# Performance work log

Hardware: AMD Instinct MI355X
Metric: run time of the kernel (lower is better)

Reference implementation:

```python
import jax, jax.numpy as jnp
import numpy as np

B, N_UNITS, SEQ, H = 4, 1024, 2048, 8
D_HEAD = N_UNITS // H
SCALE = 1.0 / D_HEAD ** 0.5


def setup_inputs() -> dict:
    key = jax.random.key(0)
    k1, k2, k3 = jax.random.split(key, 3)
    x = jax.random.normal(k1, (B, N_UNITS, SEQ), dtype=jnp.float32)
    # conv1x1 weights, bias=False; scaled like typical init
    W_qkv = jax.random.normal(k2, (3 * N_UNITS, N_UNITS), dtype=jnp.float32) * (1.0 / N_UNITS ** 0.5)
    W_out = jax.random.normal(k3, (N_UNITS, N_UNITS), dtype=jnp.float32) * (1.0 / N_UNITS ** 0.5)
    return {"x": x, "W_qkv": W_qkv, "W_out": W_out}


def reference(x, W_qkv, W_out):
    # x: (B, n_units, S). Conv1x1 == per-position linear along channel dim.
    qkv = jnp.einsum('oc,bcs->bos', W_qkv, x)          # (B, 3*n_units, S)
    Q, K, V = jnp.split(qkv, 3, axis=1)                # each (B, n_units, S)
    # torch.chunk along channels into h heads == reshape (B, h, d_head, S)
    Q = Q.reshape(B, H, D_HEAD, SEQ)
    K = K.reshape(B, H, D_HEAD, SEQ)
    V = V.reshape(B, H, D_HEAD, SEQ)
    # scores: Q^T K * scale  (NO softmax in original module; mask unused)
    A = jnp.einsum('bhdq,bhdk->bhqk', Q, K) * SCALE    # (B, h, S, S)
    # aggregation: sum_k A[q,k] * V[d,k]  (original does broadcast mul+sum)
    C = jnp.einsum('bhqk,bhdk->bhdq', A, V)            # (B, h, d_head, S)
    C = C.reshape(B, N_UNITS, SEQ)
    out = jnp.einsum('oc,bcs->bos', W_out, C)          # (B, n_units, S)
    return out
```

## Files before the change

### kernel.cpp

```cpp
#include <hip/hip_runtime.h>
#include <hip/hip_bf16.h>
#include <stdint.h>

using bf16 = __hip_bfloat16;

typedef __bf16 bf16x8 __attribute__((ext_vector_type(8)));
typedef float  f32x4  __attribute__((ext_vector_type(4)));

constexpr int Bc = 4, Hh = 8, Dh = 128, S = 2048, Cn = 1024, O3 = 3072;
constexpr float SCALE = 0.08838834764831845f;

#define GLDS16(gp, lp)                                               \
  __builtin_amdgcn_global_load_lds(                                  \
      (const __attribute__((address_space(1))) void*)(gp),           \
      (__attribute__((address_space(3))) void*)(lp), 16, 0, 0)

__device__ __forceinline__ void gemm_bt_core(
    const bf16* __restrict__ Abase, int lda,
    const bf16* __restrict__ Bbase, int ldb,
    int kIters, f32x4 (&acc)[4][4])
{
  alignas(16) __shared__ bf16 As[128 * 32];
  alignas(16) __shared__ bf16 Bs[128 * 32];
  const int t    = threadIdx.x;
  const int lane = t & 63;
  const int quad = lane >> 4, r16 = lane & 15;
  const int wave = t >> 6;
  const int wm = (wave & 1) * 64, wn = (wave >> 1) * 64;
  const int lrow = lane >> 2;
  const int lk   = (lane & 3) * 8;

  const long aOff0 = (long)(wave * 32 + lrow) * lda + lk;
  const long aOff1 = aOff0 + 16l * lda;
  const long bOff0 = (long)(wave * 32 + lrow) * ldb + lk;
  const long bOff1 = bOff0 + 16l * ldb;
  bf16* aL0 = &As[(wave * 32) * 32];
  bf16* aL1 = &As[(wave * 32 + 16) * 32];
  bf16* bL0 = &Bs[(wave * 32) * 32];
  bf16* bL1 = &Bs[(wave * 32 + 16) * 32];

#pragma unroll
  for (int i = 0; i < 4; i++)
#pragma unroll
    for (int j = 0; j < 4; j++) acc[i][j] = {0.f, 0.f, 0.f, 0.f};

  for (int ks = 0; ks < kIters; ++ks) {
    const int k0 = ks * 32;
    __syncthreads();
    GLDS16(Abase + k0 + aOff0, aL0);
    GLDS16(Abase + k0 + aOff1, aL1);
    GLDS16(Bbase + k0 + bOff0, bL0);
    GLDS16(Bbase + k0 + bOff1, bL1);
    __syncthreads();
    bf16x8 af[4], bfr[4];
#pragma unroll
    for (int i = 0; i < 4; i++)
      af[i] = *(const bf16x8*)&As[(wm + i * 16 + r16) * 32 + quad * 8];
#pragma unroll
    for (int j = 0; j < 4; j++)
      bfr[j] = *(const bf16x8*)&Bs[(wn + j * 16 + r16) * 32 + quad * 8];
#pragma unroll
    for (int i = 0; i < 4; i++)
#pragma unroll
      for (int j = 0; j < 4; j++)
        acc[i][j] = __builtin_amdgcn_mfma_f32_16x16x32_bf16(af[i], bfr[j], acc[i][j], 0, 0, 0);
  }
}

__device__ __forceinline__ void store_bf16_tile(
    f32x4 (&acc)[4][4], bf16* __restrict__ Cp, int ldc)
{
  const int t = threadIdx.x;
  const int lane = t & 63;
  const int quad = lane >> 4, r16 = lane & 15;
  const int wave = t >> 6;
  const int wm = (wave & 1) * 64, wn = (wave >> 1) * 64;
#pragma unroll
  for (int i = 0; i < 4; i++)
#pragma unroll
    for (int j = 0; j < 4; j++)
#pragma unroll
      for (int r = 0; r < 4; r++) {
        const int row = wm + i * 16 + quad * 4 + r;
        const int col = wn + j * 16 + r16;
        Cp[(long)row * ldc + col] = __float2bfloat16(acc[i][j][r]);
      }
}

__device__ __forceinline__ void store_f32_tile(
    f32x4 (&acc)[4][4], float* __restrict__ Cp, int ldc)
{
  const int t = threadIdx.x;
  const int lane = t & 63;
  const int quad = lane >> 4, r16 = lane & 15;
  const int wave = t >> 6;
  const int wm = (wave & 1) * 64, wn = (wave >> 1) * 64;
#pragma unroll
  for (int i = 0; i < 4; i++)
#pragma unroll
    for (int j = 0; j < 4; j++)
#pragma unroll
      for (int r = 0; r < 4; r++) {
        const int row = wm + i * 16 + quad * 4 + r;
        const int col = wn + j * 16 + r16;
        Cp[(long)row * ldc + col] = acc[i][j][r];
      }
}

__global__ __launch_bounds__(256) void k_cvt_w(
    const float* __restrict__ Wqkv, const float* __restrict__ Wout,
    bf16* __restrict__ WqkvB, bf16* __restrict__ WoutB)
{
  const long v = (long)blockIdx.x * 256 + threadIdx.x;
  const bool isQ = v < 786432;
  const float4 f = isQ ? ((const float4*)Wqkv)[v] : ((const float4*)Wout)[v - 786432];
  bf16 tmp[4];
  tmp[0] = __float2bfloat16(f.x);
  tmp[1] = __float2bfloat16(f.y);
  tmp[2] = __float2bfloat16(f.z);
  tmp[3] = __float2bfloat16(f.w);
  ushort4 u = *(ushort4*)tmp;
  if (isQ) ((ushort4*)WqkvB)[v] = u;
  else     ((ushort4*)WoutB)[v - 786432] = u;
}

__global__ __launch_bounds__(256) void k_transpose_cvt(
    const float* __restrict__ in, bf16* __restrict__ out, long inZ, long outZ)
{
  __shared__ bf16 tile[32][33];
  const float* ip = in + (long)blockIdx.z * inZ;
  bf16* op = out + (long)blockIdx.z * outZ;
  const int c0 = blockIdx.x * 32, r0 = blockIdx.y * 32;
  const int tx = threadIdx.x & 31, ty = threadIdx.x >> 5;
#pragma unroll
  for (int i = 0; i < 32; i += 8)
    tile[ty + i][tx] = __float2bfloat16(ip[(long)(r0 + ty + i) * 2048 + c0 + tx]);
  __syncthreads();
#pragma unroll
  for (int i = 0; i < 32; i += 8)
    op[(long)(c0 + ty + i) * 1024 + r0 + tx] = tile[tx][ty + i];
}

__global__ __launch_bounds__(256) void k_gemm_qT(
    const bf16* __restrict__ xT, const bf16* __restrict__ WqkvB, bf16* __restrict__ QT)
{
  const int m0 = blockIdx.x * 128, n0 = blockIdx.y * 128, b = blockIdx.z;
  f32x4 acc[4][4];
  gemm_bt_core(xT + (long)b * S * Cn + (long)m0 * Cn, Cn,
               WqkvB + (long)n0 * Cn, Cn, Cn / 32, acc);
  store_bf16_tile(acc, QT + (long)b * S * Cn + (long)m0 * Cn + n0, Cn);
}

__global__ __launch_bounds__(256) void k_gemm_kv(
    const bf16* __restrict__ WqkvB, const bf16* __restrict__ xT, bf16* __restrict__ KV)
{
  const int m0 = blockIdx.x * 128, n0 = blockIdx.y * 128, b = blockIdx.z;
  f32x4 acc[4][4];
  gemm_bt_core(WqkvB + (long)(Cn + m0) * Cn, Cn,
               xT + (long)b * S * Cn + (long)n0 * Cn, Cn, Cn / 32, acc);
  store_bf16_tile(acc, KV + (long)b * 2048 * S + (long)m0 * S + n0, S);
}

__global__ __launch_bounds__(256) void k_gemm_mt(
    const bf16* __restrict__ KV, float* __restrict__ MTpart)
{
  const int chunk = blockIdx.x;
  const int z = blockIdx.y;
  const int b = z >> 3, h = z & 7;
  const bf16* base = KV + (long)b * 2048 * S;
  const bf16* A  = base + (long)(h * Dh) * S + chunk * 256;
  const bf16* Bp = base + (long)(1024 + h * Dh) * S + chunk * 256;
  f32x4 acc[4][4];
  gemm_bt_core(A, S, Bp, S, 8, acc);
  store_f32_tile(acc, MTpart + ((long)chunk * 32 + z) * (Dh * Dh), Dh);
}

__global__ __launch_bounds__(256) void k_reduce_mt(
    const float* __restrict__ MTpart, bf16* __restrict__ MbT)
{
  const long i = (long)blockIdx.x * 256 + threadIdx.x;
  float s = 0.f;
#pragma unroll
  for (int c = 0; c < 8; c++) s += MTpart[(long)c * 32 * Dh * Dh + i];
  MbT[i] = __float2bfloat16(s * SCALE);
}

__global__ __launch_bounds__(256) void k_gemm_w2(
    const bf16* __restrict__ WoutB, const bf16* __restrict__ MbT, bf16* __restrict__ W2)
{
  const int m0 = blockIdx.x * 128;
  const int h = blockIdx.y, b = blockIdx.z;
  const int z = b * 8 + h;
  f32x4 acc[4][4];
  gemm_bt_core(WoutB + (long)m0 * Cn + h * Dh, Cn,
               MbT + (long)z * Dh * Dh, Dh, 4, acc);
  store_bf16_tile(acc, W2 + (long)b * Cn * Cn + (long)m0 * Cn + h * Dh, Cn);
}

__global__ __launch_bounds__(256) void k_gemm_out(
    const bf16* __restrict__ W2, const bf16* __restrict__ QT, float* __restrict__ out)
{
  const int m0 = blockIdx.x * 128, n0 = blockIdx.y * 128, b = blockIdx.z;
  f32x4 acc[4][4];
  gemm_bt_core(W2 + (long)b * Cn * Cn + (long)m0 * Cn, Cn,
               QT + (long)b * S * Cn + (long)n0 * Cn, Cn, Cn / 32, acc);
  store_f32_tile(acc, out + (long)b * Cn * S + (long)m0 * S + n0, S);
}

extern "C" void kernel_launch(void* const* d_in, const int* in_sizes, int n_in,
                              void* d_out, int out_size, void* d_ws, size_t ws_size,
                              hipStream_t stream)
{
  const float* x    = (const float*)d_in[0];
  const float* Wqkv = (const float*)d_in[1];
  const float* Wout = (const float*)d_in[2];
  float* out = (float*)d_out;

  char* ws = (char*)d_ws;
  bf16*  KV     = (bf16*)ws;
  bf16*  xT     = (bf16*)(ws + 33554432);
  float* MTpart = (float*)(ws + 33554432);
  bf16*  QT     = (bf16*)(ws + 50331648);
  bf16*  WqkvB  = (bf16*)(ws + 67108864);
  bf16*  WoutB  = (bf16*)(ws + 73400320);
  bf16*  MbT    = (bf16*)(ws + 75497472);
  bf16*  W2     = (bf16*)(ws + 76546048);

  k_cvt_w<<<dim3(4096), 256, 0, stream>>>(Wqkv, Wout, WqkvB, WoutB);
  k_transpose_cvt<<<dim3(64, 32, 4), 256, 0, stream>>>(
      x, xT, (long)1024 * 2048, (long)2048 * 1024);
  k_gemm_qT<<<dim3(16, 8, 4), 256, 0, stream>>>(xT, WqkvB, QT);
  k_gemm_kv<<<dim3(16, 16, 4), 256, 0, stream>>>(WqkvB, xT, KV);
  k_gemm_mt<<<dim3(8, 32), 256, 0, stream>>>(KV, MTpart);
  k_reduce_mt<<<dim3(2048), 256, 0, stream>>>(MTpart, MbT);
  k_gemm_w2<<<dim3(8, 8, 4), 256, 0, stream>>>(WoutB, MbT, W2);
  k_gemm_out<<<dim3(8, 16, 4), 256, 0, stream>>>(W2, QT, out);
}
```

Baseline: 221.8 us.

## Reassociate attention chain through input Gram matrix to avoid materializing K, V, Q

Replaces the explicit Q/K/V projections with an algebraic reassociation. The per-batch Gram matrix G = x x^T is computed first, then K V^T is formed per head as Wk G Wv^T, and Wout·M is folded with Wq into one per-batch 1024x1024 weight W3 that multiplies x directly. The aim is to cut the large S-dimension GEMMs and the KV intermediate traffic, and to drop the split-K partial-sum reduction kernel. In exchange it adds extra small weight-side GEMMs and rounds G, P and W3 to bf16, which may change accuracy.

```diff
diff --git a/kernel.cpp b/kernel.cpp
--- a/kernel.cpp
+++ b/kernel.cpp
@@ -7,7 +7,7 @@
 typedef __bf16 bf16x8 __attribute__((ext_vector_type(8)));
 typedef float  f32x4  __attribute__((ext_vector_type(4)));
 
-constexpr int Bc = 4, Hh = 8, Dh = 128, S = 2048, Cn = 1024, O3 = 3072;
+constexpr int Dh = 128, S = 2048, Cn = 1024;
 constexpr float SCALE = 0.08838834764831845f;
 
 #define GLDS16(gp, lp)                                               \
@@ -68,7 +68,7 @@
 }
 
 __device__ __forceinline__ void store_bf16_tile(
-    f32x4 (&acc)[4][4], bf16* __restrict__ Cp, int ldc)
+    f32x4 (&acc)[4][4], bf16* __restrict__ Cp, int ldc, float mul = 1.0f)
 {
   const int t = threadIdx.x;
   const int lane = t & 63;
@@ -83,7 +83,7 @@
       for (int r = 0; r < 4; r++) {
         const int row = wm + i * 16 + quad * 4 + r;
         const int col = wn + j * 16 + r16;
-        Cp[(long)row * ldc + col] = __float2bfloat16(acc[i][j][r]);
+        Cp[(long)row * ldc + col] = __float2bfloat16(acc[i][j][r] * mul);
       }
 }
 
@@ -109,80 +109,88 @@
 
 __global__ __launch_bounds__(256) void k_cvt_w(
     const float* __restrict__ Wqkv, const float* __restrict__ Wout,
-    bf16* __restrict__ WqkvB, bf16* __restrict__ WoutB)
+    bf16* __restrict__ WkvB, bf16* __restrict__ WoutB)
 {
   const long v = (long)blockIdx.x * 256 + threadIdx.x;
-  const bool isQ = v < 786432;
-  const float4 f = isQ ? ((const float4*)Wqkv)[v] : ((const float4*)Wout)[v - 786432];
+  const bool isKV = v < 524288;
+  const float4 f = isKV ? ((const float4*)(Wqkv + (long)Cn * Cn))[v]
+                        : ((const float4*)Wout)[v - 524288];
   bf16 tmp[4];
   tmp[0] = __float2bfloat16(f.x);
   tmp[1] = __float2bfloat16(f.y);
   tmp[2] = __float2bfloat16(f.z);
   tmp[3] = __float2bfloat16(f.w);
   ushort4 u = *(ushort4*)tmp;
-  if (isQ) ((ushort4*)WqkvB)[v] = u;
-  else     ((ushort4*)WoutB)[v - 786432] = u;
-}
-
-__global__ __launch_bounds__(256) void k_transpose_cvt(
-    const float* __restrict__ in, bf16* __restrict__ out, long inZ, long outZ)
+  if (isKV) ((ushort4*)WkvB)[v] = u;
+  else      ((ushort4*)WoutB)[v - 524288] = u;
+}
+
+__global__ __launch_bounds__(256) void k_prep_x(
+    const float* __restrict__ x, const float* __restrict__ Wqkv,
+    bf16* __restrict__ xc, bf16* __restrict__ xT, bf16* __restrict__ WqT)
 {
   __shared__ bf16 tile[32][33];
-  const float* ip = in + (long)blockIdx.z * inZ;
-  bf16* op = out + (long)blockIdx.z * outZ;
-  const int c0 = blockIdx.x * 32, r0 = blockIdx.y * 32;
   const int tx = threadIdx.x & 31, ty = threadIdx.x >> 5;
-#pragma unroll
-  for (int i = 0; i < 32; i += 8)
-    tile[ty + i][tx] = __float2bfloat16(ip[(long)(r0 + ty + i) * 2048 + c0 + tx]);
-  __syncthreads();
-#pragma unroll
-  for (int i = 0; i < 32; i += 8)
-    op[(long)(c0 + ty + i) * 1024 + r0 + tx] = tile[tx][ty + i];
-}
-
-__global__ __launch_bounds__(256) void k_gemm_qT(
-    const bf16* __restrict__ xT, const bf16* __restrict__ WqkvB, bf16* __restrict__ QT)
+  const int z = blockIdx.z;
+  if (z < 4) {
+    const float* ip = x + (long)z * Cn * S;
+    bf16* oc = xc + (long)z * Cn * S;
+    bf16* ot = xT + (long)z * S * Cn;
+    const int c0 = blockIdx.x * 32, r0 = blockIdx.y * 32;
+#pragma unroll
+    for (int i = 0; i < 32; i += 8) {
+      bf16 vb = __float2bfloat16(ip[(long)(r0 + ty + i) * S + c0 + tx]);
+      oc[(long)(r0 + ty + i) * S + c0 + tx] = vb;
+      tile[ty + i][tx] = vb;
+    }
+    __syncthreads();
+#pragma unroll
+    for (int i = 0; i < 32; i += 8)
+      ot[(long)(c0 + ty + i) * Cn + r0 + tx] = tile[tx][ty + i];
+  } else {
+    if (blockIdx.x >= 32) return;
+    const int c0 = blockIdx.x * 32, r0 = blockIdx.y * 32;
+#pragma unroll
+    for (int i = 0; i < 32; i += 8)
+      tile[ty + i][tx] = __float2bfloat16(Wqkv[(long)(r0 + ty + i) * Cn + c0 + tx]);
+    __syncthreads();
+#pragma unroll
+    for (int i = 0; i < 32; i += 8)
+      WqT[(long)(c0 + ty + i) * Cn + r0 + tx] = tile[tx][ty + i];
+  }
+}
+
+__global__ __launch_bounds__(256) void k_gemm_g(
+    const bf16* __restrict__ xc, bf16* __restrict__ G)
 {
   const int m0 = blockIdx.x * 128, n0 = blockIdx.y * 128, b = blockIdx.z;
-  f32x4 acc[4][4];
-  gemm_bt_core(xT + (long)b * S * Cn + (long)m0 * Cn, Cn,
-               WqkvB + (long)n0 * Cn, Cn, Cn / 32, acc);
-  store_bf16_tile(acc, QT + (long)b * S * Cn + (long)m0 * Cn + n0, Cn);
-}
-
-__global__ __launch_bounds__(256) void k_gemm_kv(
-    const bf16* __restrict__ WqkvB, const bf16* __restrict__ xT, bf16* __restrict__ KV)
-{
-  const int m0 = blockIdx.x * 128, n0 = blockIdx.y * 128, b = blockIdx.z;
-  f32x4 acc[4][4];
-  gemm_bt_core(WqkvB + (long)(Cn + m0) * Cn, Cn,
-               xT + (long)b * S * Cn + (long)n0 * Cn, Cn, Cn / 32, acc);
-  store_bf16_tile(acc, KV + (long)b * 2048 * S + (long)m0 * S + n0, S);
-}
-
-__global__ __launch_bounds__(256) void k_gemm_mt(
-    const bf16* __restrict__ KV, float* __restrict__ MTpart)
-{
-  const int chunk = blockIdx.x;
+  const bf16* xb = xc + (long)b * Cn * S;
+  f32x4 acc[4][4];
+  gemm_bt_core(xb + (long)m0 * S, S, xb + (long)n0 * S, S, S / 32, acc);
+  store_bf16_tile(acc, G + (long)b * Cn * Cn + (long)m0 * Cn + n0, Cn);
+}
+
+__global__ __launch_bounds__(256) void k_gemm_p(
+    const bf16* __restrict__ WkvB, const bf16* __restrict__ G, bf16* __restrict__ P)
+{
+  const int n0 = blockIdx.x * 128;
   const int z = blockIdx.y;
   const int b = z >> 3, h = z & 7;
-  const bf16* base = KV + (long)b * 2048 * S;
-  const bf16* A  = base + (long)(h * Dh) * S + chunk * 256;
-  const bf16* Bp = base + (long)(1024 + h * Dh) * S + chunk * 256;
-  f32x4 acc[4][4];
-  gemm_bt_core(A, S, Bp, S, 8, acc);
-  store_f32_tile(acc, MTpart + ((long)chunk * 32 + z) * (Dh * Dh), Dh);
-}
-
-__global__ __launch_bounds__(256) void k_reduce_mt(
-    const float* __restrict__ MTpart, bf16* __restrict__ MbT)
-{
-  const long i = (long)blockIdx.x * 256 + threadIdx.x;
-  float s = 0.f;
-#pragma unroll
-  for (int c = 0; c < 8; c++) s += MTpart[(long)c * 32 * Dh * Dh + i];
-  MbT[i] = __float2bfloat16(s * SCALE);
+  f32x4 acc[4][4];
+  gemm_bt_core(WkvB + (long)(h * Dh) * Cn, Cn,
+               G + (long)b * Cn * Cn + (long)n0 * Cn, Cn, Cn / 32, acc);
+  store_bf16_tile(acc, P + (long)z * Dh * Cn + n0, Cn);
+}
+
+__global__ __launch_bounds__(256) void k_gemm_mt(
+    const bf16* __restrict__ P, const bf16* __restrict__ WkvB, bf16* __restrict__ MbT)
+{
+  const int z = blockIdx.x;
+  const int h = z & 7;
+  f32x4 acc[4][4];
+  gemm_bt_core(P + (long)z * Dh * Cn, Cn,
+               WkvB + (long)(Cn + h * Dh) * Cn, Cn, Cn / 32, acc);
+  store_bf16_tile(acc, MbT + (long)z * Dh * Dh, Dh, SCALE);
 }
 
 __global__ __launch_bounds__(256) void k_gemm_w2(
@@ -197,13 +205,23 @@
   store_bf16_tile(acc, W2 + (long)b * Cn * Cn + (long)m0 * Cn + h * Dh, Cn);
 }
 
+__global__ __launch_bounds__(256) void k_gemm_w3(
+    const bf16* __restrict__ W2, const bf16* __restrict__ WqT, bf16* __restrict__ W3)
+{
+  const int m0 = blockIdx.x * 128, n0 = blockIdx.y * 128, b = blockIdx.z;
+  f32x4 acc[4][4];
+  gemm_bt_core(W2 + (long)b * Cn * Cn + (long)m0 * Cn, Cn,
+               WqT + (long)n0 * Cn, Cn, Cn / 32, acc);
+  store_bf16_tile(acc, W3 + (long)b * Cn * Cn + (long)m0 * Cn + n0, Cn);
+}
+
 __global__ __launch_bounds__(256) void k_gemm_out(
-    const bf16* __restrict__ W2, const bf16* __restrict__ QT, float* __restrict__ out)
+    const bf16* __restrict__ W3, const bf16* __restrict__ xT, float* __restrict__ out)
 {
   const int m0 = blockIdx.x * 128, n0 = blockIdx.y * 128, b = blockIdx.z;
   f32x4 acc[4][4];
-  gemm_bt_core(W2 + (long)b * Cn * Cn + (long)m0 * Cn, Cn,
-               QT + (long)b * S * Cn + (long)n0 * Cn, Cn, Cn / 32, acc);
+  gemm_bt_core(W3 + (long)b * Cn * Cn + (long)m0 * Cn, Cn,
+               xT + (long)b * S * Cn + (long)n0 * Cn, Cn, Cn / 32, acc);
   store_f32_tile(acc, out + (long)b * Cn * S + (long)m0 * S + n0, S);
 }
 
@@ -217,22 +235,23 @@
   float* out = (float*)d_out;
 
   char* ws = (char*)d_ws;
-  bf16*  KV     = (bf16*)ws;
-  bf16*  xT     = (bf16*)(ws + 33554432);
-  float* MTpart = (float*)(ws + 33554432);
-  bf16*  QT     = (bf16*)(ws + 50331648);
-  bf16*  WqkvB  = (bf16*)(ws + 67108864);
-  bf16*  WoutB  = (bf16*)(ws + 73400320);
-  bf16*  MbT    = (bf16*)(ws + 75497472);
-  bf16*  W2     = (bf16*)(ws + 76546048);
-
-  k_cvt_w<<<dim3(4096), 256, 0, stream>>>(Wqkv, Wout, WqkvB, WoutB);
-  k_transpose_cvt<<<dim3(64, 32, 4), 256, 0, stream>>>(
-      x, xT, (long)1024 * 2048, (long)2048 * 1024);
-  k_gemm_qT<<<dim3(16, 8, 4), 256, 0, stream>>>(xT, WqkvB, QT);
-  k_gemm_kv<<<dim3(16, 16, 4), 256, 0, stream>>>(WqkvB, xT, KV);
-  k_gemm_mt<<<dim3(8, 32), 256, 0, stream>>>(KV, MTpart);
-  k_reduce_mt<<<dim3(2048), 256, 0, stream>>>(MTpart, MbT);
+  bf16* xc    = (bf16*)ws;
+  bf16* xT    = (bf16*)(ws + 16777216);
+  bf16* G     = (bf16*)(ws + 33554432);
+  bf16* P     = (bf16*)(ws + 41943040);
+  bf16* WkvB  = (bf16*)(ws + 50331648);
+  bf16* WoutB = (bf16*)(ws + 54525952);
+  bf16* WqT   = (bf16*)(ws + 56623104);
+  bf16* MbT   = (bf16*)(ws + 58720256);
+  bf16* W2    = (bf16*)(ws + 59768832);
+  bf16* W3    = (bf16*)(ws + 68157440);
+
+  k_cvt_w<<<dim3(3072), 256, 0, stream>>>(Wqkv, Wout, WkvB, WoutB);
+  k_prep_x<<<dim3(64, 32, 5), 256, 0, stream>>>(x, Wqkv, xc, xT, WqT);
+  k_gemm_g<<<dim3(8, 8, 4), 256, 0, stream>>>(xc, G);
+  k_gemm_p<<<dim3(8, 32), 256, 0, stream>>>(WkvB, G, P);
+  k_gemm_mt<<<dim3(32), 256, 0, stream>>>(P, WkvB, MbT);
   k_gemm_w2<<<dim3(8, 8, 4), 256, 0, stream>>>(WoutB, MbT, W2);
-  k_gemm_out<<<dim3(8, 16, 4), 256, 0, stream>>>(W2, QT, out);
-}
+  k_gemm_w3<<<dim3(8, 8, 4), 256, 0, stream>>>(W2, WqT, W3);
+  k_gemm_out<<<dim3(8, 16, 4), 256, 0, stream>>>(W3, xT, out);
+}
```

New measurement: 237.4 us. 7.0% more time.
